# Performance work log

Measured on AMD Instinct MI355X. Metric: run time of the kernel, lower is better.

The kernel has to match this reference:

```python
import jax, jax.numpy as jnp
import numpy as np

N = 12                      # matrix size (input_size)
TRI = N * (N + 1) // 2      # 78 lower-triangular entries
HID = 512
BATCH = 262144


def setup_inputs() -> dict:
    key = jax.random.key(0)
    ks = jax.random.split(key, 4)
    s1 = 1.0 / np.sqrt(N)
    s2 = 1.0 / np.sqrt(HID)
    return {
        "x": jax.random.normal(ks[0], (BATCH, N), dtype=jnp.float32),
        "W1": jax.random.normal(ks[1], (N, HID), dtype=jnp.float32) * s1,
        "b1": jnp.zeros((HID,), dtype=jnp.float32),
        "W2": jax.random.normal(ks[2], (HID, HID), dtype=jnp.float32) * s2,
        "b2": jnp.zeros((HID,), dtype=jnp.float32),
        "W3": jax.random.normal(ks[3], (HID, TRI + 1), dtype=jnp.float32) * s2,
        "b3": jnp.zeros((TRI + 1,), dtype=jnp.float32),
    }


def reference(x, W1, b1, W2, b2, W3, b3):
    # 3-layer MLP (assumed parent-class structure): relu, relu, softplus
    h = jax.nn.relu(x @ W1 + b1)
    h = jax.nn.relu(h @ W2 + b2)
    out = jax.nn.softplus(h @ W3 + b3)          # [B, TRI+1]
    # Vectorized row-major lower-triangular scatter (replaces nested python loop)
    rows, cols = jnp.tril_indices(N)            # row-major order matches idx loop
    B = x.shape[0]
    L = jnp.zeros((B, N, N), dtype=out.dtype).at[:, rows, cols].set(out[:, :TRI])
    MMT = jnp.einsum('bij,bkj->bik', L, L)      # M @ M^T, PSD [B, N, N]
    c = out[:, TRI]                             # [B]
    return MMT, c
```

## Files before the change

### kernel.cpp

```cpp
#include <hip/hip_runtime.h>
#include <math.h>

typedef __attribute__((ext_vector_type(8))) _Float16 fp16x8;
typedef __attribute__((ext_vector_type(4))) _Float16 fp16x4;
typedef __attribute__((ext_vector_type(4))) float floatx4;

#define HID 512
#define TRIC 78
#define OUTC 79
#define BATCH 262144
#define HPAD 520
#define OPAD 84
#define MPAD 148
#define ML_OFF 6144
#define XPAD 24
#define X_OFF 33280

#define W2P_OFF 16384
#define W3P_OFF 278528

__global__ __launch_bounds__(256) void prep_kernel(const float* __restrict__ W1,
                                                   const float* __restrict__ W2,
                                                   const float* __restrict__ W3,
                                                   _Float16* __restrict__ wsh) {
  int g = blockIdx.x * 256 + threadIdx.x;
  int lane = g & 63;
  int l15 = lane & 15, q = lane >> 4;
  fp16x8 v;
  if (g < 2048) {
    int ct = g >> 6;
    int c = ct * 16 + l15;
#pragma unroll
    for (int j = 0; j < 8; ++j) {
      int k = q * 8 + j;
      v[j] = (k < 12) ? (_Float16)W1[k * HID + c] : (_Float16)0.f;
    }
    *(fp16x8*)(wsh + (size_t)g * 8) = v;
  } else if (g < 34816) {
    int h = g - 2048;
    int fk = h >> 6;
    int kb = fk & 15, ct = fk >> 4;
    int c = ct * 16 + l15;
    int kbase = kb * 32 + q * 8;
#pragma unroll
    for (int j = 0; j < 8; ++j) v[j] = (_Float16)W2[(kbase + j) * HID + c];
    *(fp16x8*)(wsh + W2P_OFF + (size_t)h * 8) = v;
  } else if (g < 39936) {
    int h = g - 34816;
    int fk = h >> 6;
    int kb = fk & 15, ct = fk >> 4;
    int c = ct * 16 + l15;
    int kbase = kb * 32 + q * 8;
#pragma unroll
    for (int j = 0; j < 8; ++j)
      v[j] = (c < OUTC) ? (_Float16)W3[(kbase + j) * OUTC + c] : (_Float16)0.f;
    *(fp16x8*)(wsh + W3P_OFF + (size_t)h * 8) = v;
  }
}

__device__ __forceinline__ float softplus_f(float v) {
  float e = __expf(-fabsf(v));
  return fmaxf(v, 0.f) + __logf(1.f + e);
}

__global__ __launch_bounds__(512, 4) void fused_kernel(const float* __restrict__ x,
                                                       const float* __restrict__ b1,
                                                       const float* __restrict__ b2,
                                                       const float* __restrict__ b3,
                                                       const _Float16* __restrict__ wsh,
                                                       float* __restrict__ out) {
  __shared__ __align__(16) _Float16 hbuf[X_OFF + 64 * XPAD];
  const int tid = threadIdx.x;
  const int wave = tid >> 6, lane = tid & 63;
  const int l15 = lane & 15, quad = lane >> 4;
  const int r0 = blockIdx.x * 64;

  {
    _Float16* xs = hbuf + X_OFF;
    const float* xg = x + (size_t)r0 * 12;
    if (tid < 256) {
      int e = 512 + tid;
      int row = e / 12, col = e - row * 12;
      xs[row * XPAD + col] = (_Float16)xg[e];
      xs[(tid >> 2) * XPAD + 12 + (tid & 3)] = (_Float16)0.f;
    }
    {
      int row = tid / 12, col = tid - row * 12;
      xs[row * XPAD + col] = (_Float16)xg[tid];
    }
  }
  __syncthreads();

  const fp16x8* w1p = (const fp16x8*)wsh;
  const fp16x8* w2p = (const fp16x8*)(wsh + W2P_OFF);
  const fp16x8* w3p = (const fp16x8*)(wsh + W3P_OFF);

  fp16x8 zf;
#pragma unroll
  for (int j = 0; j < 8; ++j) zf[j] = (_Float16)0.f;

  floatx4 bq[4];
#pragma unroll
  for (int ct = 0; ct < 4; ++ct)
    bq[ct] = *(const floatx4*)(b1 + wave * 64 + ct * 16 + quad * 4);

  floatx4 acc[4][4];
#pragma unroll
  for (int ct = 0; ct < 4; ++ct)
#pragma unroll
    for (int nt = 0; nt < 4; ++nt) acc[ct][nt] = bq[ct];

  {
    const _Float16* xs = hbuf + X_OFF;
    fp16x8 xb[4];
#pragma unroll
    for (int nt = 0; nt < 4; ++nt)
      xb[nt] = (quad < 2) ? *(const fp16x8*)(xs + (nt * 16 + l15) * XPAD + quad * 8) : zf;
#pragma unroll
    for (int ct = 0; ct < 4; ++ct) {
      fp16x8 a1 = w1p[(wave * 4 + ct) * 64 + lane];
#pragma unroll
      for (int nt = 0; nt < 4; ++nt)
        acc[ct][nt] = __builtin_amdgcn_mfma_f32_16x16x32_f16(a1, xb[nt], acc[ct][nt], 0, 0, 0);
    }
  }

#pragma unroll
  for (int ct = 0; ct < 4; ++ct)
#pragma unroll
    for (int nt = 0; nt < 4; ++nt) {
      fp16x4 p;
#pragma unroll
      for (int r = 0; r < 4; ++r) p[r] = (_Float16)fmaxf(acc[ct][nt][r], 0.f);
      *(fp16x4*)(hbuf + (nt * 16 + l15) * HPAD + wave * 64 + ct * 16 + quad * 4) = p;
    }
  __syncthreads();

#pragma unroll
  for (int ct = 0; ct < 4; ++ct)
    bq[ct] = *(const floatx4*)(b2 + wave * 64 + ct * 16 + quad * 4);
#pragma unroll
  for (int ct = 0; ct < 4; ++ct)
#pragma unroll
    for (int nt = 0; nt < 4; ++nt) acc[ct][nt] = bq[ct];

#pragma unroll 2
  for (int kb = 0; kb < 16; ++kb) {
    fp16x8 a[4], b[4];
#pragma unroll
    for (int ct = 0; ct < 4; ++ct) a[ct] = w2p[((wave * 4 + ct) * 16 + kb) * 64 + lane];
#pragma unroll
    for (int nt = 0; nt < 4; ++nt)
      b[nt] = *(const fp16x8*)(hbuf + (nt * 16 + l15) * HPAD + kb * 32 + quad * 8);
    __builtin_amdgcn_s_setprio(1);
#pragma unroll
    for (int ct = 0; ct < 4; ++ct)
#pragma unroll
      for (int nt = 0; nt < 4; ++nt)
        acc[ct][nt] = __builtin_amdgcn_mfma_f32_16x16x32_f16(a[ct], b[nt], acc[ct][nt], 0, 0, 0);
    __builtin_amdgcn_s_setprio(0);
  }

  __syncthreads();

#pragma unroll
  for (int ct = 0; ct < 4; ++ct)
#pragma unroll
    for (int nt = 0; nt < 4; ++nt) {
      fp16x4 p;
#pragma unroll
      for (int r = 0; r < 4; ++r) p[r] = (_Float16)fmaxf(acc[ct][nt][r], 0.f);
      *(fp16x4*)(hbuf + (nt * 16 + l15) * HPAD + wave * 64 + ct * 16 + quad * 4) = p;
    }
  __syncthreads();

  const int mt3 = wave >> 1;
  const int codd = wave & 1;
  const int c0 = codd ? 3 : 0;
  const int nct = codd ? 2 : 3;

  floatx4 b3q[3];
#pragma unroll
  for (int j = 0; j < 3; ++j) {
#pragma unroll
    for (int r = 0; r < 4; ++r) {
      int c = (c0 + j) * 16 + quad * 4 + r;
      b3q[j][r] = (j < nct && c < OUTC) ? b3[c] : 0.f;
    }
  }
  floatx4 acc3[3];
#pragma unroll
  for (int j = 0; j < 3; ++j) acc3[j] = b3q[j];

#pragma unroll 2
  for (int kb = 0; kb < 16; ++kb) {
    fp16x8 bfrag = *(const fp16x8*)(hbuf + (mt3 * 16 + l15) * HPAD + kb * 32 + quad * 8);
    __builtin_amdgcn_s_setprio(1);
#pragma unroll
    for (int j = 0; j < 3; ++j)
      if (j < nct)
        acc3[j] = __builtin_amdgcn_mfma_f32_16x16x32_f16(
            w3p[((c0 + j) * 16 + kb) * 64 + lane], bfrag, acc3[j], 0, 0, 0);
    __builtin_amdgcn_s_setprio(0);
  }
  __syncthreads();

  float* outf = (float*)hbuf;
#pragma unroll
  for (int j = 0; j < 3; ++j)
    if (j < nct) {
      floatx4 v;
#pragma unroll
      for (int r = 0; r < 4; ++r) v[r] = softplus_f(acc3[j][r]);
      *(floatx4*)(outf + (mt3 * 16 + l15) * OPAD + (c0 + j) * 16 + quad * 4) = v;
    }
  __syncthreads();

  {
    const float* Lbase = (const float*)hbuf;
    float* Mbase = (float*)hbuf + ML_OFF;
    const int rowl = tid >> 3;
    const int sub = tid & 7;
    const float* Lr = Lbase + rowl * OPAD;

    float R[80];
#pragma unroll
    for (int q = 0; q < 20; ++q) {
      floatx4 v = *(const floatx4*)(Lr + q * 4);
#pragma unroll
      for (int r = 0; r < 4; ++r) R[q * 4 + r] = v[r];
    }

    float Lj0[12], Lj1[12];
    {
      const int tj = (sub * (sub + 1)) >> 1;
#pragma unroll
      for (int k = 0; k < 12; ++k) Lj0[k] = (k <= sub) ? Lr[tj + k] : 0.f;
#pragma unroll
      for (int k = 0; k < 12; ++k) Lj1[k] = 0.f;
      const int j1 = sub + 8;
      if (sub < 4) {
        const int tj1 = (j1 * (j1 + 1)) >> 1;
#pragma unroll
        for (int k = 0; k < 12; ++k) Lj1[k] = (k <= j1) ? Lr[tj1 + k] : 0.f;
      }
    }

    float* Mr = Mbase + rowl * MPAD;
#pragma unroll
    for (int i = 0; i < 12; ++i) {
      const int ti = (i * (i + 1)) >> 1;
      float s0 = 0.f, s1 = 0.f;
#pragma unroll
      for (int k = 0; k <= i; ++k) {
        const float li = R[ti + k];
        s0 = fmaf(li, Lj0[k], s0);
        s1 = fmaf(li, Lj1[k], s1);
      }
      Mr[i * 12 + sub] = s0;
      if (sub < 4) Mr[i * 12 + sub + 8] = s1;
    }
  }
  __syncthreads();

  {
    const float* Mbase = (const float*)hbuf + ML_OFF;
    float* og = out + (size_t)r0 * 144;
#pragma unroll
    for (int s = 0; s < 4; ++s) {
      int e4 = tid + s * 512;
      int row = e4 / 36, c4 = e4 - row * 36;
      *(floatx4*)(og + row * 144 + c4 * 4) = *(const floatx4*)(Mbase + row * MPAD + c4 * 4);
    }
    if (tid < 256) {
      int e4 = 2048 + tid;
      int row = e4 / 36, c4 = e4 - row * 36;
      *(floatx4*)(og + row * 144 + c4 * 4) = *(const floatx4*)(Mbase + row * MPAD + c4 * 4);
    }
    if (tid < 64) {
      const float* Lbase = (const float*)hbuf;
      out[(size_t)BATCH * 144 + r0 + tid] = Lbase[tid * OPAD + TRIC];
    }
  }
}

extern "C" void kernel_launch(void* const* d_in, const int* in_sizes, int n_in,
                              void* d_out, int out_size, void* d_ws, size_t ws_size,
                              hipStream_t stream) {
  const float* x  = (const float*)d_in[0];
  const float* W1 = (const float*)d_in[1];
  const float* b1 = (const float*)d_in[2];
  const float* W2 = (const float*)d_in[3];
  const float* b2 = (const float*)d_in[4];
  const float* W3 = (const float*)d_in[5];
  const float* b3 = (const float*)d_in[6];
  float* out = (float*)d_out;
  _Float16* wsh = (_Float16*)d_ws;

  prep_kernel<<<156, 256, 0, stream>>>(W1, W2, W3, wsh);
  fused_kernel<<<BATCH / 64, 512, 0, stream>>>(x, b1, b2, b3, wsh, out);
}
```

Baseline: 329.8 us.

## Prefetch weight fragments ahead of MFMA loops and store PSD output directly to global

Weight fragments for layers 1-3 are loaded one iteration ahead (software pipelining) so global/L2 latency overlaps the MFMA work and the preceding barriers. A redundant barrier after the layer-2 activation writeback is removed by folding it into the prefetch. The M·Mᵀ result is written straight to global memory instead of staged through LDS, which removes one barrier and an LDS round trip. The c column is written directly from registers. Direct global stores are scalar and strided (12 floats per row split across 8 threads), which may coalesce worse than the earlier float4 copy.

```diff
diff --git a/kernel.cpp b/kernel.cpp
--- a/kernel.cpp
+++ b/kernel.cpp
@@ -11,8 +11,6 @@
 #define BATCH 262144
 #define HPAD 520
 #define OPAD 84
-#define MPAD 148
-#define ML_OFF 6144
 #define XPAD 24
 #define X_OFF 33280
 
@@ -75,6 +73,10 @@
   const int l15 = lane & 15, quad = lane >> 4;
   const int r0 = blockIdx.x * 64;
 
+  const fp16x8* w1p = (const fp16x8*)wsh;
+  const fp16x8* w2p = (const fp16x8*)(wsh + W2P_OFF);
+  const fp16x8* w3p = (const fp16x8*)(wsh + W3P_OFF);
+
   {
     _Float16* xs = hbuf + X_OFF;
     const float* xg = x + (size_t)r0 * 12;
@@ -89,11 +91,10 @@
       xs[row * XPAD + col] = (_Float16)xg[tid];
     }
   }
-  __syncthreads();
-
-  const fp16x8* w1p = (const fp16x8*)wsh;
-  const fp16x8* w2p = (const fp16x8*)(wsh + W2P_OFF);
-  const fp16x8* w3p = (const fp16x8*)(wsh + W3P_OFF);
+  fp16x8 a1p[4];
+#pragma unroll
+  for (int ct = 0; ct < 4; ++ct) a1p[ct] = w1p[(wave * 4 + ct) * 64 + lane];
+  __syncthreads();
 
   fp16x8 zf;
 #pragma unroll
@@ -118,10 +119,9 @@
       xb[nt] = (quad < 2) ? *(const fp16x8*)(xs + (nt * 16 + l15) * XPAD + quad * 8) : zf;
 #pragma unroll
     for (int ct = 0; ct < 4; ++ct) {
-      fp16x8 a1 = w1p[(wave * 4 + ct) * 64 + lane];
 #pragma unroll
       for (int nt = 0; nt < 4; ++nt)
-        acc[ct][nt] = __builtin_amdgcn_mfma_f32_16x16x32_f16(a1, xb[nt], acc[ct][nt], 0, 0, 0);
+        acc[ct][nt] = __builtin_amdgcn_mfma_f32_16x16x32_f16(a1p[ct], xb[nt], acc[ct][nt], 0, 0, 0);
     }
   }
 
@@ -134,6 +134,9 @@
       for (int r = 0; r < 4; ++r) p[r] = (_Float16)fmaxf(acc[ct][nt][r], 0.f);
       *(fp16x4*)(hbuf + (nt * 16 + l15) * HPAD + wave * 64 + ct * 16 + quad * 4) = p;
     }
+  fp16x8 ap[4];
+#pragma unroll
+  for (int ct = 0; ct < 4; ++ct) ap[ct] = w2p[((wave * 4 + ct) * 16 + 0) * 64 + lane];
   __syncthreads();
 
 #pragma unroll
@@ -148,10 +151,13 @@
   for (int kb = 0; kb < 16; ++kb) {
     fp16x8 a[4], b[4];
 #pragma unroll
-    for (int ct = 0; ct < 4; ++ct) a[ct] = w2p[((wave * 4 + ct) * 16 + kb) * 64 + lane];
+    for (int ct = 0; ct < 4; ++ct) a[ct] = ap[ct];
 #pragma unroll
     for (int nt = 0; nt < 4; ++nt)
       b[nt] = *(const fp16x8*)(hbuf + (nt * 16 + l15) * HPAD + kb * 32 + quad * 8);
+    const int kbn = (kb + 1) & 15;
+#pragma unroll
+    for (int ct = 0; ct < 4; ++ct) ap[ct] = w2p[((wave * 4 + ct) * 16 + kbn) * 64 + lane];
     __builtin_amdgcn_s_setprio(1);
 #pragma unroll
     for (int ct = 0; ct < 4; ++ct)
@@ -172,7 +178,6 @@
       for (int r = 0; r < 4; ++r) p[r] = (_Float16)fmaxf(acc[ct][nt][r], 0.f);
       *(fp16x4*)(hbuf + (nt * 16 + l15) * HPAD + wave * 64 + ct * 16 + quad * 4) = p;
     }
-  __syncthreads();
 
   const int mt3 = wave >> 1;
   const int codd = wave & 1;
@@ -192,15 +197,29 @@
 #pragma unroll
   for (int j = 0; j < 3; ++j) acc3[j] = b3q[j];
 
+  fp16x8 ap3[3];
+#pragma unroll
+  for (int j = 0; j < 3; ++j) ap3[j] = zf;
+#pragma unroll
+  for (int j = 0; j < 3; ++j)
+    if (j < nct) ap3[j] = w3p[((c0 + j) * 16 + 0) * 64 + lane];
+  __syncthreads();
+
 #pragma unroll 2
   for (int kb = 0; kb < 16; ++kb) {
     fp16x8 bfrag = *(const fp16x8*)(hbuf + (mt3 * 16 + l15) * HPAD + kb * 32 + quad * 8);
+    fp16x8 a3[3];
+#pragma unroll
+    for (int j = 0; j < 3; ++j) a3[j] = ap3[j];
+    const int kbn = (kb + 1) & 15;
+#pragma unroll
+    for (int j = 0; j < 3; ++j)
+      if (j < nct) ap3[j] = w3p[((c0 + j) * 16 + kbn) * 64 + lane];
     __builtin_amdgcn_s_setprio(1);
 #pragma unroll
     for (int j = 0; j < 3; ++j)
       if (j < nct)
-        acc3[j] = __builtin_amdgcn_mfma_f32_16x16x32_f16(
-            w3p[((c0 + j) * 16 + kb) * 64 + lane], bfrag, acc3[j], 0, 0, 0);
+        acc3[j] = __builtin_amdgcn_mfma_f32_16x16x32_f16(a3[j], bfrag, acc3[j], 0, 0, 0);
     __builtin_amdgcn_s_setprio(0);
   }
   __syncthreads();
@@ -214,11 +233,12 @@
       for (int r = 0; r < 4; ++r) v[r] = softplus_f(acc3[j][r]);
       *(floatx4*)(outf + (mt3 * 16 + l15) * OPAD + (c0 + j) * 16 + quad * 4) = v;
     }
+  if (codd && quad == 3)
+    out[(size_t)BATCH * 144 + r0 + mt3 * 16 + l15] = softplus_f(acc3[1][2]);
   __syncthreads();
 
   {
     const float* Lbase = (const float*)hbuf;
-    float* Mbase = (float*)hbuf + ML_OFF;
     const int rowl = tid >> 3;
     const int sub = tid & 7;
     const float* Lr = Lbase + rowl * OPAD;
@@ -246,7 +266,7 @@
       }
     }
 
-    float* Mr = Mbase + rowl * MPAD;
+    float* Mg = out + ((size_t)r0 + rowl) * 144;
 #pragma unroll
     for (int i = 0; i < 12; ++i) {
       const int ti = (i * (i + 1)) >> 1;
@@ -257,29 +277,8 @@
         s0 = fmaf(li, Lj0[k], s0);
         s1 = fmaf(li, Lj1[k], s1);
       }
-      Mr[i * 12 + sub] = s0;
-      if (sub < 4) Mr[i * 12 + sub + 8] = s1;
-    }
-  }
-  __syncthreads();
-
-  {
-    const float* Mbase = (const float*)hbuf + ML_OFF;
-    float* og = out + (size_t)r0 * 144;
-#pragma unroll
-    for (int s = 0; s < 4; ++s) {
-      int e4 = tid + s * 512;
-      int row = e4 / 36, c4 = e4 - row * 36;
-      *(floatx4*)(og + row * 144 + c4 * 4) = *(const floatx4*)(Mbase + row * MPAD + c4 * 4);
-    }
-    if (tid < 256) {
-      int e4 = 2048 + tid;
-      int row = e4 / 36, c4 = e4 - row * 36;
-      *(floatx4*)(og + row * 144 + c4 * 4) = *(const floatx4*)(Mbase + row * MPAD + c4 * 4);
-    }
-    if (tid < 64) {
-      const float* Lbase = (const float*)hbuf;
-      out[(size_t)BATCH * 144 + r0 + tid] = Lbase[tid * OPAD + TRIC];
+      Mg[i * 12 + sub] = s0;
+      if (sub < 4) Mg[i * 12 + sub + 8] = s1;
     }
   }
 }
```

Measured after the change: 329.6 us. About the same (-0.1%).
